# Kernel tuning notes

Hardware: AMD Instinct MI355X
Metric: run time of the kernel (lower is better)

The kernel has to match this reference:

```python
import jax, jax.numpy as jnp
import numpy as np
from math import sqrt

D_MODEL = 1024
N_HEADS = 16
FF_MULT = 4
MAX_DIST = 512
LN_EPS = 1e-5


def layer_norm(x, g, b):
    mu = jnp.mean(x, axis=-1, keepdims=True)
    var = jnp.var(x, axis=-1, keepdims=True)
    return (x - mu) * jax.lax.rsqrt(var + LN_EPS) * g + b


def setup_inputs() -> dict:
    key = jax.random.key(0)
    ks = jax.random.split(key, 10)
    D, H, F = D_MODEL, N_HEADS, D_MODEL * FF_MULT
    s = 0.02
    return {
        "x": jax.random.normal(ks[0], (2, 2048, D), dtype=jnp.float32),
        "w_qkv": jax.random.normal(ks[1], (D, 3 * D), dtype=jnp.float32) * s,
        "b_qkv": jnp.zeros((3 * D,), jnp.float32),
        "w_out": jax.random.normal(ks[2], (D, D), dtype=jnp.float32) * s,
        "b_out": jnp.zeros((D,), jnp.float32),
        "rel_bias": jax.random.normal(ks[3], (2 * MAX_DIST + 1, H), dtype=jnp.float32) * s,
        "g1": jnp.ones((D,), jnp.float32),
        "beta1": jnp.zeros((D,), jnp.float32),
        "w1": jax.random.normal(ks[4], (D, F), dtype=jnp.float32) * s,
        "b1": jnp.zeros((F,), jnp.float32),
        "w2": jax.random.normal(ks[5], (F, D), dtype=jnp.float32) * s,
        "b2": jnp.zeros((D,), jnp.float32),
        "g2": jnp.ones((D,), jnp.float32),
        "beta2": jnp.zeros((D,), jnp.float32),
    }


def reference(x, w_qkv, b_qkv, w_out, b_out, rel_bias, g1, beta1, w1, b1, w2, b2, g2, beta2):
    B, T, D = x.shape
    H = N_HEADS
    hd = D // H
    qkv = x @ w_qkv + b_qkv                      # [B,T,3D]
    q, k, v = jnp.split(qkv, 3, axis=-1)
    # [B,H,T,hd]
    q = q.reshape(B, T, H, hd).transpose(0, 2, 1, 3)
    k = k.reshape(B, T, H, hd).transpose(0, 2, 1, 3)
    v = v.reshape(B, T, H, hd).transpose(0, 2, 1, 3)
    scores = jnp.einsum("bhqd,bhkd->bhqk", q, k) / sqrt(hd)
    # relative position bias: gather from table [2*max_dist+1, H]
    rel = jnp.clip(jnp.arange(T)[None, :] - jnp.arange(T)[:, None], -MAX_DIST, MAX_DIST) + MAX_DIST
    bias = rel_bias[rel].transpose(2, 0, 1)       # [H,T,T]
    attn = jax.nn.softmax(scores + bias[None], axis=-1)
    out = jnp.einsum("bhqk,bhkd->bhqd", attn, v).transpose(0, 2, 1, 3).reshape(B, T, D)
    out = out @ w_out + b_out                     # dropout inactive (eval)
    x2 = layer_norm(x + out, g1, beta1)
    ff = jax.nn.gelu(x2 @ w1 + b1, approximate=False) @ w2 + b2
    x3 = layer_norm(x2 + ff, g2, beta2)
    return (x3, attn)
```

## Files before the change

### kernel.cpp

```cpp
#include <hip/hip_runtime.h>
#include <hip/hip_bf16.h>
#include <cstdint>
#include <cstddef>

#define DEVFN static __device__ __forceinline__

typedef __attribute__((ext_vector_type(8))) short bf16x8;
typedef __attribute__((ext_vector_type(4))) float f32x4;

#define WAITVM(N) asm volatile("s_waitcnt vmcnt(" #N ")" ::: "memory")
#define WAITLGKM() asm volatile("s_waitcnt lgkmcnt(0)" ::: "memory")
#define BAR() __builtin_amdgcn_s_barrier()

DEVFN float exp2f_fast(float x) { return __builtin_amdgcn_exp2f(x); }

DEVFN ushort f2bf(float f) {
  uint32_t u = __float_as_uint(f);
  return (ushort)((u + 0x7fffu + ((u >> 16) & 1u)) >> 16);
}

DEVFN void gl_lds16(const void* g, void* l) {
  __builtin_amdgcn_global_load_lds(
      (const __attribute__((address_space(1))) void*)g,
      (__attribute__((address_space(3))) void*)l, 16, 0, 0);
}

DEVFN float wred_sum(float v) {
#pragma unroll
  for (int o = 32; o; o >>= 1) v += __shfl_xor(v, o);
  return v;
}


__global__ __launch_bounds__(256) void pack_bf16(const float* __restrict__ in,
                                                 ushort* __restrict__ out) {
  size_t i = ((size_t)blockIdx.x * 256 + threadIdx.x) * 4;
  float4 v = *(const float4*)&in[i];
  ushort4 u = make_ushort4(f2bf(v.x), f2bf(v.y), f2bf(v.z), f2bf(v.w));
  *(ushort4*)&out[i] = u;
}

__global__ __launch_bounds__(256) void wtrans(const float* __restrict__ in,
                                              ushort* __restrict__ out,
                                              int K, int N) {
  __shared__ float tile[32][33];
  int n0 = blockIdx.x * 32, k0 = blockIdx.y * 32;
  int tid = threadIdx.x;
#pragma unroll
  for (int i = 0; i < 4; ++i) {
    int idx = tid + i * 256;
    int r = idx >> 5, c = idx & 31;
    tile[r][c] = in[(size_t)(k0 + r) * N + n0 + c];
  }
  __syncthreads();
#pragma unroll
  for (int i = 0; i < 4; ++i) {
    int idx = tid + i * 256;
    int r = idx >> 5, c = idx & 31;
    out[(size_t)(n0 + r) * K + k0 + c] = f2bf(tile[c][r]);
  }
}

__global__ __launch_bounds__(256) void pack_vT(const ushort* __restrict__ qkv,
                                               ushort* __restrict__ vT) {
  __shared__ ushort tile[64][72];
  int bh = blockIdx.y, b = bh >> 4, h = bh & 15;
  int t0 = blockIdx.x * 64;
  int tid = threadIdx.x;
#pragma unroll
  for (int i = 0; i < 16; ++i) {
    int idx = tid + i * 256;
    int r = idx >> 6, c = idx & 63;
    tile[r][c] = qkv[(size_t)(b * 2048 + t0 + r) * 3072 + 2048 + h * 64 + c];
  }
  __syncthreads();
#pragma unroll
  for (int i = 0; i < 16; ++i) {
    int idx = tid + i * 256;
    int d = idx >> 6, t = idx & 63;
    vT[((size_t)bh * 64 + d) * 2048 + t0 + t] = tile[t][d];
  }
}


template <bool GELU, bool STF32, bool STBF16>
__global__ __launch_bounds__(256)
void gemm128(const ushort* __restrict__ A, int lda,
             const ushort* __restrict__ BT, int ldb,
             const float* __restrict__ bias,
             float* __restrict__ Cf, ushort* __restrict__ Cb, int ldc, int K,
             size_t cstride) {
  __shared__ ushort lsa[128 * 64];
  __shared__ ushort lsb[128 * 64];
  const int tid = threadIdx.x;
  const int lane = tid & 63;
  const int wv = tid >> 6;
  const int wr = (wv >> 1) * 64, wc = (wv & 1) * 64;
  const size_t kStart = (size_t)blockIdx.z * K;
  const ushort* Ab = A + (size_t)blockIdx.y * 128 * lda + kStart;
  const ushort* Bb = BT + (size_t)blockIdx.x * 128 * ldb + kStart;
  f32x4 acc[4][4] = {};
  int rowS[4], slotS[4];
#pragma unroll
  for (int i = 0; i < 4; ++i) {
    int idx = tid + i * 256;
    rowS[i] = idx >> 3;
    slotS[i] = (idx & 7) ^ (rowS[i] & 7);
  }
  for (int kt = 0; kt < K; kt += 64) {
    __syncthreads();
#pragma unroll
    for (int i = 0; i < 4; ++i) {
      gl_lds16(Ab + (size_t)rowS[i] * lda + kt + slotS[i] * 8, &lsa[(tid + i * 256) * 8]);
      gl_lds16(Bb + (size_t)rowS[i] * ldb + kt + slotS[i] * 8, &lsb[(tid + i * 256) * 8]);
    }
    asm volatile("s_waitcnt vmcnt(0)" ::: "memory");
    __syncthreads();
#pragma unroll
    for (int kk = 0; kk < 2; ++kk) {
      bf16x8 af[4], bfr[4];
      const int g = kk * 4 + (lane >> 4);
#pragma unroll
      for (int m = 0; m < 4; ++m) {
        int r = wr + m * 16 + (lane & 15);
        af[m] = *(const bf16x8*)&lsa[r * 64 + ((g ^ (r & 7)) * 8)];
      }
#pragma unroll
      for (int n = 0; n < 4; ++n) {
        int r = wc + n * 16 + (lane & 15);
        bfr[n] = *(const bf16x8*)&lsb[r * 64 + ((g ^ (r & 7)) * 8)];
      }
#pragma unroll
      for (int m = 0; m < 4; ++m)
#pragma unroll
        for (int n = 0; n < 4; ++n)
          acc[m][n] = __builtin_amdgcn_mfma_f32_16x16x32_bf16(af[m], bfr[n], acc[m][n], 0, 0, 0);
    }
  }
  const int rb = blockIdx.y * 128 + wr + ((lane >> 4) << 2);
  const int cb = blockIdx.x * 128 + wc + (lane & 15);
  float* Cfz = Cf + (size_t)blockIdx.z * cstride;
  ushort* Cbz = Cb + (size_t)blockIdx.z * cstride;
#pragma unroll
  for (int m = 0; m < 4; ++m)
#pragma unroll
    for (int n = 0; n < 4; ++n) {
      int col = cb + n * 16;
      float bv = bias ? bias[col] : 0.0f;
#pragma unroll
      for (int i = 0; i < 4; ++i) {
        int row = rb + m * 16 + i;
        float v = acc[m][n][i] + bv;
        if (GELU) v = 0.5f * v * (1.0f + erff(v * 0.70710678f));
        if (STF32) Cfz[(size_t)row * ldc + col] = v;
        if (STBF16) Cbz[(size_t)row * ldc + col] = f2bf(v);
      }
    }
}


DEVFN void attn_bid(int& qb, int& bh) {
  int lin = blockIdx.x;
  int xcd = lin & 7;
  int idx = lin >> 3;
  int orig = xcd * 64 + idx;
  qb = orig & 15;
  bh = orig >> 4;
}

__global__ __launch_bounds__(256, 4)
void attn_den(const ushort* __restrict__ qkv, const float* __restrict__ rel_bias,
              float* __restrict__ invl) {
  __shared__ ushort lsk[2][64 * 64];
  __shared__ float extb[1034];
  const int tid = threadIdx.x;
  const int lane = tid & 63;
  const int wv = tid >> 6;
  const int hi = lane >> 4;
  const int lo = lane & 15;
  int qb, bh;
  attn_bid(qb, bh);
  const int b = bh >> 4, h = bh & 15;
  const int q0 = qb * 128;
  const ushort* qp = qkv + (size_t)b * 2048 * 3072 + h * 64;
  const ushort* kp = qp + 1024;
  const float C_SC = 0.18033688011f;
  ushort* lsq = (ushort*)lsk;

  for (int i = tid; i < 1034; i += 256) {
    int j = i - 3;
    j = j < 0 ? 0 : (j > 1024 ? 1024 : j);
    extb[i] = rel_bias[j * 16 + h] * 1.44269504f;
  }
#pragma unroll
  for (int i = 0; i < 4; ++i) {
    int idx = tid + i * 256;
    int row = idx >> 3;
    int slot = (idx & 7) ^ (row & 7);
    gl_lds16(qp + (size_t)(q0 + row) * 3072 + slot * 8, &lsq[idx * 8]);
  }
  WAITVM(0);
  WAITLGKM();
  BAR();
  bf16x8 qf[2][2];
#pragma unroll
  for (int mq = 0; mq < 2; ++mq)
#pragma unroll
    for (int kk = 0; kk < 2; ++kk) {
      int r = wv * 32 + mq * 16 + lo;
      int g = kk * 4 + hi;
      qf[mq][kk] = *(const bf16x8*)&lsq[r * 64 + ((g ^ (r & 7)) * 8)];
    }
  WAITLGKM();
  BAR();

  const int r0 = tid >> 3;
  const int sl0 = (tid & 7) ^ (r0 & 7);
  const int r1 = (tid + 256) >> 3;
  const int sl1 = ((tid + 256) & 7) ^ (r1 & 7);
  auto stageK = [&](int t, int buf) {
    gl_lds16(kp + (size_t)(t * 64 + r0) * 3072 + sl0 * 8, &lsk[buf][tid * 8]);
    gl_lds16(kp + (size_t)(t * 64 + r1) * 3072 + sl1 * 8, &lsk[buf][(tid + 256) * 8]);
  };

  float l_part[2] = {0.0f, 0.0f};
  stageK(0, 0);
  for (int t = 0; t < 32; ++t) {
    if (t < 31) {
      stageK(t + 1, (t + 1) & 1);
      WAITVM(2);
    } else {
      WAITVM(0);
    }
    BAR();
    f32x4 sacc[4][2] = {};
    __builtin_amdgcn_s_setprio(1);
#pragma unroll
    for (int kk = 0; kk < 2; ++kk) {
      const int g = kk * 4 + hi;
      bf16x8 ak[4];
#pragma unroll
      for (int mk = 0; mk < 4; ++mk) {
        int r = mk * 16 + lo;
        ak[mk] = *(const bf16x8*)&lsk[t & 1][r * 64 + ((g ^ (r & 7)) * 8)];
      }
#pragma unroll
      for (int mk = 0; mk < 4; ++mk)
#pragma unroll
        for (int mq = 0; mq < 2; ++mq)
          sacc[mk][mq] =
              __builtin_amdgcn_mfma_f32_16x16x32_bf16(ak[mk], qf[mq][kk], sacc[mk][mq], 0, 0, 0);
    }
    __builtin_amdgcn_s_setprio(0);
    const bool farR = (t * 64) >= q0 + 640;
    const bool farL = (t * 64 + 63) <= q0 - 512;
    if (farR || farL) {
      const float bc = farR ? extb[3 + 1024] : extb[3];
#pragma unroll
      for (int mq = 0; mq < 2; ++mq) {
        float s = 0.0f;
#pragma unroll
        for (int mk = 0; mk < 4; ++mk)
#pragma unroll
          for (int i = 0; i < 4; ++i)
            s += exp2f_fast(fmaf(sacc[mk][mq][i], C_SC, bc));
        l_part[mq] += s;
      }
    } else {
      const int kbase = t * 64 + hi * 4;
      const int qr = q0 + wv * 32 + lo;
#pragma unroll
      for (int mq = 0; mq < 2; ++mq) {
        float s = 0.0f;
#pragma unroll
        for (int mk = 0; mk < 4; ++mk) {
          int k0 = (kbase + mk * 16) - (qr + mq * 16) + 515;
          k0 = k0 < 0 ? 0 : (k0 > 1030 ? 1030 : k0);
#pragma unroll
          for (int i = 0; i < 4; ++i)
            s += exp2f_fast(fmaf(sacc[mk][mq][i], C_SC, extb[k0 + i]));
        }
        l_part[mq] += s;
      }
    }
    BAR();
  }

#pragma unroll
  for (int mq = 0; mq < 2; ++mq) {
    float l = l_part[mq];
    l += __shfl_xor(l, 16);
    l += __shfl_xor(l, 32);
    if (hi == 0)
      invl[(size_t)bh * 2048 + q0 + wv * 32 + mq * 16 + lo] = 1.0f / l;
  }
}

__global__ __launch_bounds__(256, 3)
void attn_pv2(const ushort* __restrict__ qkv, const ushort* __restrict__ vT,
              const float* __restrict__ rel_bias, const float* __restrict__ invl,
              float* __restrict__ attn, ushort* __restrict__ ctx) {
  __shared__ ushort lsk[2][64 * 64];
  __shared__ ushort lsv[2][64 * 64];
  __shared__ ushort lsp[128 * 64];
  __shared__ float extb[1034];
  const int tid = threadIdx.x;
  const int lane = tid & 63;
  const int wv = tid >> 6;
  const int hi = lane >> 4;
  const int lo = lane & 15;
  int qb, bh;
  attn_bid(qb, bh);
  const int b = bh >> 4, h = bh & 15;
  const int q0 = qb * 128;
  const ushort* qp = qkv + (size_t)b * 2048 * 3072 + h * 64;
  const ushort* kp = qp + 1024;
  const ushort* vp = vT + (size_t)bh * 64 * 2048;
  float* attnb = attn + (size_t)bh * 2048 * 2048;
  const float C_SC = 0.18033688011f;

  for (int i = tid; i < 1034; i += 256) {
    int j = i - 3;
    j = j < 0 ? 0 : (j > 1024 ? 1024 : j);
    extb[i] = rel_bias[j * 16 + h] * 1.44269504f;
  }
#pragma unroll
  for (int i = 0; i < 4; ++i) {
    int idx = tid + i * 256;
    int row = idx >> 3;
    int slot = (idx & 7) ^ (row & 7);
    gl_lds16(qp + (size_t)(q0 + row) * 3072 + slot * 8, &lsp[idx * 8]);
  }
  WAITVM(0);
  WAITLGKM();
  BAR();
  bf16x8 qf[2][2];
#pragma unroll
  for (int mq = 0; mq < 2; ++mq)
#pragma unroll
    for (int kk = 0; kk < 2; ++kk) {
      int r = wv * 32 + mq * 16 + lo;
      int g = kk * 4 + hi;
      qf[mq][kk] = *(const bf16x8*)&lsp[r * 64 + ((g ^ (r & 7)) * 8)];
    }
  WAITLGKM();
  BAR();

  float il[2];
#pragma unroll
  for (int mq = 0; mq < 2; ++mq)
    il[mq] = invl[(size_t)bh * 2048 + q0 + wv * 32 + mq * 16 + lo];

  const int r0 = tid >> 3;
  const int sl0 = (tid & 7) ^ (r0 & 7);
  const int r1 = (tid + 256) >> 3;
  const int sl1 = ((tid + 256) & 7) ^ (r1 & 7);
  auto stageK = [&](int t, int buf) {
    gl_lds16(kp + (size_t)(t * 64 + r0) * 3072 + sl0 * 8, &lsk[buf][tid * 8]);
    gl_lds16(kp + (size_t)(t * 64 + r1) * 3072 + sl1 * 8, &lsk[buf][(tid + 256) * 8]);
  };
  auto stageV = [&](int t, int buf) {
    gl_lds16(vp + (size_t)r0 * 2048 + t * 64 + sl0 * 8, &lsv[buf][tid * 8]);
    gl_lds16(vp + (size_t)r1 * 2048 + t * 64 + sl1 * 8, &lsv[buf][(tid + 256) * 8]);
  };

  f32x4 acc_o[2][4] = {};
  stageK(0, 0);
  stageV(0, 0);
  for (int t = 0; t < 32; ++t) {
    if (t < 31) {
      stageK(t + 1, (t + 1) & 1);
      stageV(t + 1, (t + 1) & 1);
    }
    if (t == 0) { WAITVM(4); }
    else if (t < 31) { WAITVM(12); }
    else { WAITVM(8); }
    BAR();
    f32x4 sacc[4][2] = {};
    __builtin_amdgcn_s_setprio(1);
#pragma unroll
    for (int kk = 0; kk < 2; ++kk) {
      const int g = kk * 4 + hi;
      bf16x8 ak[4];
#pragma unroll
      for (int mk = 0; mk < 4; ++mk) {
        int r = mk * 16 + lo;
        ak[mk] = *(const bf16x8*)&lsk[t & 1][r * 64 + ((g ^ (r & 7)) * 8)];
      }
#pragma unroll
      for (int mk = 0; mk < 4; ++mk)
#pragma unroll
        for (int mq = 0; mq < 2; ++mq)
          sacc[mk][mq] =
              __builtin_amdgcn_mfma_f32_16x16x32_bf16(ak[mk], qf[mq][kk], sacc[mk][mq], 0, 0, 0);
    }
    __builtin_amdgcn_s_setprio(0);
    const bool farR = (t * 64) >= q0 + 640;
    const bool farT = farR || ((t * 64 + 63) <= q0 - 512);
    const float bcf = farR ? extb[3 + 1024] : extb[3];
#pragma unroll
    for (int mq = 0; mq < 2; ++mq) {
      const int row = wv * 32 + mq * 16 + lo;
      const float l = il[mq];
#pragma unroll
      for (int mk = 0; mk < 4; ++mk) {
        const int c0 = mk * 16 + hi * 4;
        float p4[4];
        if (farT) {
#pragma unroll
          for (int i = 0; i < 4; ++i)
            p4[i] = exp2f_fast(fmaf(sacc[mk][mq][i], C_SC, bcf)) * l;
        } else {
          int k0 = (t * 64 + c0) - (q0 + row) + 515;
          k0 = k0 < 0 ? 0 : (k0 > 1030 ? 1030 : k0);
#pragma unroll
          for (int i = 0; i < 4; ++i)
            p4[i] = exp2f_fast(fmaf(sacc[mk][mq][i], C_SC, extb[k0 + i])) * l;
        }
        ushort4 u = make_ushort4(f2bf(p4[0]), f2bf(p4[1]), f2bf(p4[2]), f2bf(p4[3]));
        *(ushort4*)&lsp[row * 64 + (((c0 >> 3) ^ (row & 7)) << 3) + (c0 & 7)] = u;
        *(float4*)&attnb[(size_t)(q0 + row) * 2048 + t * 64 + c0] =
            make_float4(p4[0], p4[1], p4[2], p4[3]);
      }
    }
    WAITLGKM();
    BAR();
    __builtin_amdgcn_s_setprio(1);
#pragma unroll
    for (int kk = 0; kk < 2; ++kk) {
      const int g = kk * 4 + hi;
      bf16x8 ap[2], bv2[4];
#pragma unroll
      for (int m = 0; m < 2; ++m) {
        int r = wv * 32 + m * 16 + lo;
        ap[m] = *(const bf16x8*)&lsp[r * 64 + ((g ^ (r & 7)) * 8)];
      }
#pragma unroll
      for (int n = 0; n < 4; ++n) {
        int r = n * 16 + lo;
        bv2[n] = *(const bf16x8*)&lsv[t & 1][r * 64 + ((g ^ (r & 7)) * 8)];
      }
#pragma unroll
      for (int m = 0; m < 2; ++m)
#pragma unroll
        for (int n = 0; n < 4; ++n)
          acc_o[m][n] = __builtin_amdgcn_mfma_f32_16x16x32_bf16(ap[m], bv2[n], acc_o[m][n], 0, 0, 0);
    }
    __builtin_amdgcn_s_setprio(0);
  }

#pragma unroll
  for (int m = 0; m < 2; ++m)
#pragma unroll
    for (int n = 0; n < 4; ++n) {
      int col = h * 64 + n * 16 + lo;
#pragma unroll
      for (int i = 0; i < 4; ++i) {
        int row = q0 + wv * 32 + m * 16 + (hi << 2) + i;
        ctx[(size_t)(b * 2048 + row) * 1024 + col] = f2bf(acc_o[m][n][i]);
      }
    }
}


__global__ __launch_bounds__(256)
void add_ln(const float* __restrict__ a, const float* __restrict__ r0,
            const float* __restrict__ r1, const float* __restrict__ bias,
            const float* __restrict__ g, const float* __restrict__ be,
            float* __restrict__ outf, ushort* __restrict__ outb) {
  const int tid = threadIdx.x;
  const size_t base = (size_t)blockIdx.x * 1024 + tid * 4;
  float4 va = *(const float4*)&a[base];
  float4 vr = *(const float4*)&r0[base];
  float x0 = va.x + vr.x, x1 = va.y + vr.y, x2 = va.z + vr.z, x3 = va.w + vr.w;
  if (r1) {
    float4 v1 = *(const float4*)&r1[base];
    x0 += v1.x; x1 += v1.y; x2 += v1.z; x3 += v1.w;
  }
  if (bias) {
    float4 vb4 = *(const float4*)&bias[tid * 4];
    x0 += vb4.x; x1 += vb4.y; x2 += vb4.z; x3 += vb4.w;
  }
  float s = x0 + x1 + x2 + x3;
  float s2 = x0 * x0 + x1 * x1 + x2 * x2 + x3 * x3;
  s = wred_sum(s);
  s2 = wred_sum(s2);
  __shared__ float rs[4], rq[4];
  if ((tid & 63) == 0) { rs[tid >> 6] = s; rq[tid >> 6] = s2; }
  __syncthreads();
  s = rs[0] + rs[1] + rs[2] + rs[3];
  s2 = rq[0] + rq[1] + rq[2] + rq[3];
  const float mean = s * (1.0f / 1024.0f);
  const float var = s2 * (1.0f / 1024.0f) - mean * mean;
  const float sc = rsqrtf(var + 1e-5f);
  float4 vg = *(const float4*)&g[tid * 4];
  float4 vb = *(const float4*)&be[tid * 4];
  float y0 = (x0 - mean) * sc * vg.x + vb.x;
  float y1 = (x1 - mean) * sc * vg.y + vb.y;
  float y2 = (x2 - mean) * sc * vg.z + vb.z;
  float y3 = (x3 - mean) * sc * vg.w + vb.w;
  *(float4*)&outf[base] = make_float4(y0, y1, y2, y3);
  if (outb) {
    ushort4 u = make_ushort4(f2bf(y0), f2bf(y1), f2bf(y2), f2bf(y3));
    *(ushort4*)&outb[base] = u;
  }
}


extern "C" void kernel_launch(void* const* d_in, const int* in_sizes, int n_in,
                              void* d_out, int out_size, void* d_ws, size_t ws_size,
                              hipStream_t stream) {
  const float* x     = (const float*)d_in[0];
  const float* w_qkv = (const float*)d_in[1];
  const float* b_qkv = (const float*)d_in[2];
  const float* w_out = (const float*)d_in[3];
  const float* b_out = (const float*)d_in[4];
  const float* relb  = (const float*)d_in[5];
  const float* g1    = (const float*)d_in[6];
  const float* be1   = (const float*)d_in[7];
  const float* w1    = (const float*)d_in[8];
  const float* b1    = (const float*)d_in[9];
  const float* w2    = (const float*)d_in[10];
  const float* b2    = (const float*)d_in[11];
  const float* g2    = (const float*)d_in[12];
  const float* be2   = (const float*)d_in[13];

  float* x3o  = (float*)d_out;
  float* attn = x3o + (size_t)4194304;

  char* w = (char*)d_ws;
  size_t off = 0;
  auto alloc = [&](size_t bytes) {
    void* p = w + off;
    off += (bytes + 255) & ~(size_t)255;
    return p;
  };
  ushort* x_bf   = (ushort*)alloc(4096ull * 1024 * 2);
  ushort* wqkvT  = (ushort*)alloc(3072ull * 1024 * 2);
  ushort* woutT  = (ushort*)alloc(1024ull * 1024 * 2);
  ushort* w1T    = (ushort*)alloc(4096ull * 1024 * 2);
  ushort* w2T    = (ushort*)alloc(1024ull * 4096 * 2);
  ushort* qkv_bf = (ushort*)alloc(4096ull * 3072 * 2);
  ushort* vT     = (ushort*)alloc(32ull * 64 * 2048 * 2);
  ushort* ctx_bf = (ushort*)alloc(4096ull * 1024 * 2);
  float*  invl   = (float*)alloc(32ull * 2048 * 4);
  float*  p0     = (float*)alloc(4096ull * 1024 * 4);
  float*  p1     = (float*)alloc(4096ull * 1024 * 4);
  float*  x2f    = (float*)alloc(4096ull * 1024 * 4);
  ushort* x2bf   = (ushort*)alloc(4096ull * 1024 * 2);
  ushort* ff1_bf = (ushort*)alloc(4096ull * 4096 * 2);

  pack_bf16<<<4096, 256, 0, stream>>>(x, x_bf);
  wtrans<<<dim3(96, 32), 256, 0, stream>>>(w_qkv, wqkvT, 1024, 3072);
  wtrans<<<dim3(32, 32), 256, 0, stream>>>(w_out, woutT, 1024, 1024);
  wtrans<<<dim3(128, 32), 256, 0, stream>>>(w1, w1T, 1024, 4096);
  wtrans<<<dim3(32, 128), 256, 0, stream>>>(w2, w2T, 4096, 1024);

  gemm128<false, false, true><<<dim3(24, 32), 256, 0, stream>>>(
      x_bf, 1024, wqkvT, 1024, b_qkv, nullptr, qkv_bf, 3072, 1024, 0);
  attn_den<<<512, 256, 0, stream>>>(qkv_bf, relb, invl);
  pack_vT<<<dim3(32, 32), 256, 0, stream>>>(qkv_bf, vT);
  attn_pv2<<<512, 256, 0, stream>>>(qkv_bf, vT, relb, invl, attn, ctx_bf);

  gemm128<false, true, false><<<dim3(8, 32, 2), 256, 0, stream>>>(
      ctx_bf, 1024, woutT, 1024, nullptr, p0, nullptr, 1024, 512,
      (size_t)(p1 - p0));
  add_ln<<<4096, 256, 0, stream>>>(x, p0, p1, b_out, g1, be1, x2f, x2bf);
  gemm128<true, false, true><<<dim3(32, 32), 256, 0, stream>>>(
      x2bf, 1024, w1T, 1024, b1, nullptr, ff1_bf, 4096, 1024, 0);
  gemm128<false, true, false><<<dim3(8, 32, 2), 256, 0, stream>>>(
      ff1_bf, 4096, w2T, 4096, nullptr, p0, nullptr, 1024, 2048,
      (size_t)(p1 - p0));
  add_ln<<<4096, 256, 0, stream>>>(x2f, p0, p1, b2, g2, be2, x3o, nullptr);
}
```

Before: 452.0 us.

## Split attention key range across two blocks per query tile

Both attention kernels now split the key dimension into two halves, so each block handles 16 key tiles instead of 32 and the grid doubles to 1024 blocks. Partial row sums are stored per half and added before inversion. Partial PV outputs are written in fp32 and summed into bf16 ctx by a new combine kernel. This targets low occupancy with only 512 blocks on 256 CUs, at the cost of re-staging Q and the bias table per block, extra fp32 partial writes (about 32MB), and an extra launch.

```diff
diff --git a/kernel.cpp b/kernel.cpp
--- a/kernel.cpp
+++ b/kernel.cpp
@@ -159,18 +159,19 @@
 }
 
 
-DEVFN void attn_bid(int& qb, int& bh) {
+DEVFN void attn_bid2(int& qb, int& bh, int& hf) {
   int lin = blockIdx.x;
   int xcd = lin & 7;
   int idx = lin >> 3;
-  int orig = xcd * 64 + idx;
-  qb = orig & 15;
-  bh = orig >> 4;
+  int orig = xcd * 128 + idx;
+  hf = orig & 1;
+  qb = (orig >> 1) & 15;
+  bh = orig >> 5;
 }
 
 __global__ __launch_bounds__(256, 4)
 void attn_den(const ushort* __restrict__ qkv, const float* __restrict__ rel_bias,
-              float* __restrict__ invl) {
+              float* __restrict__ lsum) {
   __shared__ ushort lsk[2][64 * 64];
   __shared__ float extb[1034];
   const int tid = threadIdx.x;
@@ -178,10 +179,11 @@
   const int wv = tid >> 6;
   const int hi = lane >> 4;
   const int lo = lane & 15;
-  int qb, bh;
-  attn_bid(qb, bh);
+  int qb, bh, hf;
+  attn_bid2(qb, bh, hf);
   const int b = bh >> 4, h = bh & 15;
   const int q0 = qb * 128;
+  const int t0 = hf * 16;
   const ushort* qp = qkv + (size_t)b * 2048 * 3072 + h * 64;
   const ushort* kp = qp + 1024;
   const float C_SC = 0.18033688011f;
@@ -224,9 +226,9 @@
   };
 
   float l_part[2] = {0.0f, 0.0f};
-  stageK(0, 0);
-  for (int t = 0; t < 32; ++t) {
-    if (t < 31) {
+  stageK(t0, 0);
+  for (int t = t0; t < t0 + 16; ++t) {
+    if (t < t0 + 15) {
       stageK(t + 1, (t + 1) & 1);
       WAITVM(2);
     } else {
@@ -292,14 +294,14 @@
     l += __shfl_xor(l, 16);
     l += __shfl_xor(l, 32);
     if (hi == 0)
-      invl[(size_t)bh * 2048 + q0 + wv * 32 + mq * 16 + lo] = 1.0f / l;
+      lsum[(size_t)hf * 65536 + (size_t)bh * 2048 + q0 + wv * 32 + mq * 16 + lo] = l;
   }
 }
 
 __global__ __launch_bounds__(256, 3)
 void attn_pv2(const ushort* __restrict__ qkv, const ushort* __restrict__ vT,
-              const float* __restrict__ rel_bias, const float* __restrict__ invl,
-              float* __restrict__ attn, ushort* __restrict__ ctx) {
+              const float* __restrict__ rel_bias, const float* __restrict__ lsum,
+              float* __restrict__ attn, float* __restrict__ opart) {
   __shared__ ushort lsk[2][64 * 64];
   __shared__ ushort lsv[2][64 * 64];
   __shared__ ushort lsp[128 * 64];
@@ -309,10 +311,11 @@
   const int wv = tid >> 6;
   const int hi = lane >> 4;
   const int lo = lane & 15;
-  int qb, bh;
-  attn_bid(qb, bh);
+  int qb, bh, hf;
+  attn_bid2(qb, bh, hf);
   const int b = bh >> 4, h = bh & 15;
   const int q0 = qb * 128;
+  const int t0 = hf * 16;
   const ushort* qp = qkv + (size_t)b * 2048 * 3072 + h * 64;
   const ushort* kp = qp + 1024;
   const ushort* vp = vT + (size_t)bh * 64 * 2048;
@@ -348,8 +351,10 @@
 
   float il[2];
 #pragma unroll
-  for (int mq = 0; mq < 2; ++mq)
-    il[mq] = invl[(size_t)bh * 2048 + q0 + wv * 32 + mq * 16 + lo];
+  for (int mq = 0; mq < 2; ++mq) {
+    size_t qi = (size_t)bh * 2048 + q0 + wv * 32 + mq * 16 + lo;
+    il[mq] = 1.0f / (lsum[qi] + lsum[qi + 65536]);
+  }
 
   const int r0 = tid >> 3;
   const int sl0 = (tid & 7) ^ (r0 & 7);
@@ -365,15 +370,15 @@
   };
 
   f32x4 acc_o[2][4] = {};
-  stageK(0, 0);
-  stageV(0, 0);
-  for (int t = 0; t < 32; ++t) {
-    if (t < 31) {
+  stageK(t0, 0);
+  stageV(t0, 0);
+  for (int t = t0; t < t0 + 16; ++t) {
+    if (t < t0 + 15) {
       stageK(t + 1, (t + 1) & 1);
       stageV(t + 1, (t + 1) & 1);
     }
-    if (t == 0) { WAITVM(4); }
-    else if (t < 31) { WAITVM(12); }
+    if (t == t0) { WAITVM(4); }
+    else if (t < t0 + 15) { WAITVM(12); }
     else { WAITVM(8); }
     BAR();
     f32x4 sacc[4][2] = {};
@@ -449,6 +454,7 @@
     __builtin_amdgcn_s_setprio(0);
   }
 
+  float* ob = opart + (size_t)hf * 4194304;
 #pragma unroll
   for (int m = 0; m < 2; ++m)
 #pragma unroll
@@ -457,9 +463,19 @@
 #pragma unroll
       for (int i = 0; i < 4; ++i) {
         int row = q0 + wv * 32 + m * 16 + (hi << 2) + i;
-        ctx[(size_t)(b * 2048 + row) * 1024 + col] = f2bf(acc_o[m][n][i]);
-      }
-    }
+        ob[(size_t)(b * 2048 + row) * 1024 + col] = acc_o[m][n][i];
+      }
+    }
+}
+
+__global__ __launch_bounds__(256) void ocomb(const float* __restrict__ opart,
+                                             ushort* __restrict__ ctx) {
+  size_t i = ((size_t)blockIdx.x * 256 + threadIdx.x) * 4;
+  float4 a = *(const float4*)&opart[i];
+  float4 c = *(const float4*)&opart[4194304 + i];
+  ushort4 u = make_ushort4(f2bf(a.x + c.x), f2bf(a.y + c.y),
+                           f2bf(a.z + c.z), f2bf(a.w + c.w));
+  *(ushort4*)&ctx[i] = u;
 }
 
 
@@ -543,7 +559,8 @@
   ushort* qkv_bf = (ushort*)alloc(4096ull * 3072 * 2);
   ushort* vT     = (ushort*)alloc(32ull * 64 * 2048 * 2);
   ushort* ctx_bf = (ushort*)alloc(4096ull * 1024 * 2);
-  float*  invl   = (float*)alloc(32ull * 2048 * 4);
+  float*  lsum   = (float*)alloc(2ull * 32 * 2048 * 4);
+  float*  opart  = (float*)alloc(2ull * 4096 * 1024 * 4);
   float*  p0     = (float*)alloc(4096ull * 1024 * 4);
   float*  p1     = (float*)alloc(4096ull * 1024 * 4);
   float*  x2f    = (float*)alloc(4096ull * 1024 * 4);
@@ -558,9 +575,10 @@
 
   gemm128<false, false, true><<<dim3(24, 32), 256, 0, stream>>>(
       x_bf, 1024, wqkvT, 1024, b_qkv, nullptr, qkv_bf, 3072, 1024, 0);
-  attn_den<<<512, 256, 0, stream>>>(qkv_bf, relb, invl);
+  attn_den<<<1024, 256, 0, stream>>>(qkv_bf, relb, lsum);
   pack_vT<<<dim3(32, 32), 256, 0, stream>>>(qkv_bf, vT);
-  attn_pv2<<<512, 256, 0, stream>>>(qkv_bf, vT, relb, invl, attn, ctx_bf);
+  attn_pv2<<<1024, 256, 0, stream>>>(qkv_bf, vT, relb, lsum, attn, opart);
+  ocomb<<<4096, 256, 0, stream>>>(opart, ctx_bf);
 
   gemm128<false, true, false><<<dim3(8, 32, 2), 256, 0, stream>>>(
       ctx_bf, 1024, woutT, 1024, nullptr, p0, nullptr, 1024, 512,
```

New measurement: 451.1 us. Within noise of the previous version (-0.2%).
